# Kernel tuning notes

Measured on AMD Instinct MI355X. Metric: run time of the kernel, lower is better.

Reference implementation:

```python
import jax, jax.numpy as jnp
import numpy as np

B, C, H, W = 32, 3, 512, 512
EPS = 1e-8


def _radius_bins(h, w):
    cy, cx = h // 2, w // 2
    y = jnp.arange(h, dtype=jnp.float32) - cy
    x = jnp.arange(w, dtype=jnp.float32) - cx
    radius = jnp.sqrt(y[:, None] ** 2 + x[None, :] ** 2)  # [H, W]
    max_r = min(cy, cx)
    bins = jnp.floor(radius).astype(jnp.int32)
    # pixels with radius >= max_r fall outside all bins in the original loop;
    # route them to a dummy overflow bin that we drop afterwards.
    bins = jnp.where(bins < max_r, bins, max_r)
    return bins.reshape(-1), max_r


def _psd(x):
    f = jnp.fft.fft2(x)                  # over last two dims, like torch.fft.fft2
    psd = jnp.abs(f) ** 2
    return jnp.log(psd + EPS)            # log_power=True


def _radial_average(psd):
    b, c, h, w = psd.shape
    bins, max_r = _radius_bins(h, w)     # [H*W], static
    data = psd.reshape(b * c, h * w).T   # [H*W, B*C]
    sums = jax.ops.segment_sum(data, bins, num_segments=max_r + 1)
    counts = jax.ops.segment_sum(jnp.ones((h * w,), psd.dtype), bins,
                                 num_segments=max_r + 1)
    avg = jnp.where(counts[:, None] > 0, sums / counts[:, None], 0.0)
    avg = avg[:max_r]                    # drop overflow bin -> [max_r, B*C]
    return avg.T.reshape(b, c, max_r)


def setup_inputs() -> dict:
    key = jax.random.key(0)
    k1, k2 = jax.random.split(key)
    predicted = jax.random.normal(k1, (B, C, H, W), dtype=jnp.float32)
    target = jax.random.normal(k2, (B, C, H, W), dtype=jnp.float32)
    return {"predicted": predicted, "target": target}


def reference(predicted, target):
    pred_rad = _radial_average(_psd(predicted))
    targ_rad = _radial_average(_psd(target))
    return jnp.mean(jnp.abs(pred_rad - targ_rad))  # l1, reduction='mean'
```

## Files before the change

kernel.cpp:

```cpp
#include <hip/hip_runtime.h>
#include <math.h>

#define HH 512
#define WW 512
#define IMG (HH*WW)
#define NIMG_PER 96
#define NIMG 192
#define NBIN 256
#define EPSV 1e-8f
#define LN2F 0.69314718055994530942f

#define CSTR 264
#define IMGC (512*CSTR)
#define NTILE 33
#define SLOT 575

typedef float v2f __attribute__((ext_vector_type(2)));

__device__ __forceinline__ int drev(int s) {
    return ((s & 7) << 6) | (s & 56) | (s >> 6);
}
__device__ __forceinline__ int fsw(int a) { return a + (a >> 3); }

__device__ __forceinline__ v2f cmul(v2f a, v2f b) {
    return (v2f){a.x, a.x} * b + (v2f){a.y, a.y} * (v2f){-b.y, b.x};
}
__device__ __forceinline__ v2f cni(v2f a) { return (v2f){a.y, -a.x}; }

__device__ __forceinline__ void wsync() {
    asm volatile("" ::: "memory");
    __builtin_amdgcn_wave_barrier();
    asm volatile("" ::: "memory");
}

__device__ __forceinline__ void bfly8(v2f x[8]) {
    const float R = 0.70710678118654752440f;
    v2f t0=x[0]+x[4], t4=x[0]-x[4];
    v2f t1=x[1]+x[5], t5=x[1]-x[5];
    v2f t2=x[2]+x[6], t6=x[2]-x[6];
    v2f t3=x[3]+x[7], t7=x[3]-x[7];
    v2f u0=t0+t2, u2=t0-t2;
    v2f u1=t1+t3, u3=t1-t3;
    x[0]=u0+u1; x[4]=u0-u1;
    { v2f n3 = cni(u3); x[2]=u2+n3; x[6]=u2-n3; }
    v2f s1 = (v2f){R, R} * ((v2f){t5.x, t5.y} + (v2f){t5.y, -t5.x});
    v2f s2 = cni(t6);
    v2f s3 = (v2f){R, R} * ((v2f){t7.y, -t7.x} - (v2f){t7.x, t7.y});
    v2f v0=t4+s2, v2_=t4-s2;
    v2f v1=s1+s3, v3=s1-s3;
    x[1]=v0+v1; x[5]=v0-v1;
    { v2f m3 = cni(v3); x[3]=v2_+m3; x[7]=v2_-m3; }
}

__device__ __forceinline__ void twiddle7(v2f* x, float ang) {
    const float sn = __sinf(ang), cs = __cosf(ang);
    const v2f w1 = (v2f){cs, sn};
    const v2f w2 = cmul(w1, w1);
    const v2f w3 = cmul(w2, w1);
    const v2f w4 = cmul(w2, w2);
    const v2f w5 = cmul(w2, w3);
    const v2f w6 = cmul(w3, w3);
    const v2f w7 = cmul(w3, w4);
    x[1]=cmul(x[1],w1); x[2]=cmul(x[2],w2); x[3]=cmul(x[3],w3);
    x[4]=cmul(x[4],w4); x[5]=cmul(x[5],w5); x[6]=cmul(x[6],w6);
    x[7]=cmul(x[7],w7);
}

__global__ __launch_bounds__(512) void rowfft_kernel(
    const float* __restrict__ pred, const float* __restrict__ targ,
    v2f* __restrict__ out, int img_base)
{
    __shared__ v2f sd[8*SLOT];
    const int t    = threadIdx.x;
    const int lane = t & 63;
    const int w    = t >> 6;

    const int pb = blockIdx.x;
    const int li = blockIdx.y;
    const int g  = img_base + li;
    const float* img = (g < NIMG_PER) ? (pred + (size_t)g * IMG)
                                      : (targ + (size_t)(g - NIMG_PER) * IMG);
    const float* rowA = img + (size_t)(pb*16 + 2*w) * WW + lane;
    const float* rowB = rowA + WW;

    v2f* p = sd + w * SLOT;
    v2f x[8];
    const int i = lane;

    #pragma unroll
    for (int j = 0; j < 8; ++j)
        x[j] = (v2f){rowA[64*j], rowB[64*j]};
    bfly8(x);
    twiddle7(x, -0.012271846303085130f * (float)i);
    {
        v2f* q = p + fsw(i);
        #pragma unroll
        for (int j = 0; j < 8; ++j) q[72*j] = x[j];
    }
    wsync();

    {
        v2f* q = p + 72*(i >> 3) + (i & 7);
        #pragma unroll
        for (int j = 0; j < 8; ++j) x[j] = q[9*j];
        bfly8(x);
        twiddle7(x, -0.098174770424681038f * (float)(i & 7));
        #pragma unroll
        for (int j = 0; j < 8; ++j) q[9*j] = x[j];
    }
    wsync();

    {
        v2f* q = p + 9*i;
        #pragma unroll
        for (int j = 0; j < 8; ++j) x[j] = q[j];
        bfly8(x);
        #pragma unroll
        for (int j = 0; j < 8; ++j) q[j] = x[j];
    }
    wsync();

    v2f* dstA = out + (size_t)li * IMGC + (size_t)(pb*16 + 2*w) * CSTR;
    v2f* dstB = dstA + CSTR;
    #pragma unroll
    for (int it = 0; it < 5; ++it) {
        const int k = it*64 + lane;
        if (k <= 256) {
            const v2f P = p[fsw(drev(k))];
            const v2f Q = p[fsw(drev((512 - k) & 511))];
            dstA[k] = (v2f){0.5f, 0.5f} * (P + (v2f){Q.x, -Q.y});
            dstB[k] = (v2f){0.5f, 0.5f} * ((v2f){P.y, -P.x} + (v2f){Q.y, Q.x});
        } else if (k < CSTR) {
            dstA[k] = (v2f){0.0f, 0.0f};
            dstB[k] = (v2f){0.0f, 0.0f};
        }
    }
}

__global__ __launch_bounds__(512) void colfft_kernel(
    const v2f* __restrict__ in, float* __restrict__ bins2, int img_base)
{
    __shared__ v2f sd[8*SLOT];
    __shared__ float bs[4*257];
    const int t    = threadIdx.x;
    const int lane = t & 63;
    const int w    = t >> 6;

    for (int id = t; id < 4*257; id += 512) bs[id] = 0.0f;

    const int li = blockIdx.y;
    const int x0 = blockIdx.x * 8;
    {
        const int y0  = t >> 2;
        const int clp = t & 3;
        const float4* gsrc = (const float4*)(in + (size_t)li * IMGC + x0)
                           + (size_t)y0 * (CSTR/2) + clp;
        v2f* dA = sd + (2*clp)*SLOT + fsw(y0);
        v2f* dB = dA + SLOT;
        #pragma unroll
        for (int it = 0; it < 4; ++it) {
            const float4 v = gsrc[(size_t)it * 128 * (CSTR/2)];
            dA[144*it] = (v2f){v.x, v.y};
            dB[144*it] = (v2f){v.z, v.w};
        }
    }
    __syncthreads();

    v2f* p = sd + w * SLOT;
    v2f x[8];
    const int i = lane;

    {
        v2f* q = p + fsw(i);
        #pragma unroll
        for (int j = 0; j < 8; ++j) x[j] = q[72*j];
        bfly8(x);
        twiddle7(x, -0.012271846303085130f * (float)i);
        #pragma unroll
        for (int j = 0; j < 8; ++j) q[72*j] = x[j];
    }
    wsync();

    {
        v2f* q = p + 72*(i >> 3) + (i & 7);
        #pragma unroll
        for (int j = 0; j < 8; ++j) x[j] = q[9*j];
        bfly8(x);
        twiddle7(x, -0.098174770424681038f * (float)(i & 7));
        #pragma unroll
        for (int j = 0; j < 8; ++j) q[9*j] = x[j];
    }
    wsync();

    {
        v2f* q = p + 9*i;
        #pragma unroll
        for (int j = 0; j < 8; ++j) x[j] = q[j];
        bfly8(x);
        #pragma unroll
        for (int j = 0; j < 8; ++j) q[j] = x[j];
    }
    wsync();

    {
        const int h  = lane;
        const int kx = x0 + w;
        const bool valid = (kx <= 256);
        const float scale = (kx == 0 || kx == 256) ? 0.5f : 1.0f;
        const float dxf = (float)((kx - 256) * (kx - 256));
        float* bsw = bs + (w & 3) * 257;
        v2f* qb = p + fsw(8*(h & 7) + (h >> 3));
        float dyf = (float)(8*h - 256);

        float acc = 0.0f;
        int prevb = 1000;
        #pragma unroll
        for (int j = 0; j < 8; ++j) {
            const v2f v = qb[72*j];
            const float val = __log2f(fmaf(v.x, v.x, fmaf(v.y, v.y, EPSV)));
            const int b = (int)sqrtf(fmaf(dyf, dyf, dxf));
            dyf += 1.0f;
            if (b != prevb) {
                if (prevb < NBIN && valid) atomicAdd(&bsw[prevb], acc * scale);
                prevb = b; acc = val;
            } else {
                acc += val;
            }
        }
        if (prevb < NBIN && valid) atomicAdd(&bsw[prevb], acc * scale);
    }
    __syncthreads();

    if (t < NBIN) {
        float v = 0.0f;
        #pragma unroll
        for (int r = 0; r < 4; ++r) v += bs[r*257 + t];
        bins2[((size_t)blockIdx.x * NIMG + (img_base + li)) * NBIN + t] = 2.0f * v;
    }
}

__global__ __launch_bounds__(256) void reduce_kernel(
    const float* __restrict__ bins2, float* __restrict__ bins)
{
    const int li = blockIdx.x;
    const int t  = threadIdx.x;
    float s = 0.0f;
    #pragma unroll
    for (int tile = 0; tile < NTILE; ++tile)
        s += bins2[((size_t)tile * NIMG + li) * NBIN + t];
    bins[(size_t)li * NBIN + t] = s;
}

__global__ __launch_bounds__(256) void counts_kernel(float* __restrict__ cnt)
{
    __shared__ float c[NBIN];
    const int t = threadIdx.x;
    c[t] = 0.0f;
    __syncthreads();

    const int base = blockIdx.x * 4096;
    #pragma unroll
    for (int i = 0; i < 16; ++i) {
        const int id = base + i * 256 + t;
        const int y = id >> 9, xx = id & 511;
        const int dy = y - 256, dx = xx - 256;
        const int b  = (int)sqrtf((float)(dy*dy + dx*dx));
        if (b < NBIN) atomicAdd(&c[b], 1.0f);
    }
    __syncthreads();
    if (c[t] != 0.0f) atomicAdd(&cnt[t], c[t]);
}

__global__ __launch_bounds__(256) void finalize_kernel(
    const float* __restrict__ bins, const float* __restrict__ cnt,
    float* __restrict__ out)
{
    __shared__ float red[256];
    const int t = threadIdx.x;

    float acc = 0.0f;
    for (int id = t; id < NIMG_PER * NBIN; id += 256) {
        const int i = id >> 8;
        const int r = id & 255;
        const float d = fabsf(bins[(size_t)i * NBIN + r]
                            - bins[(size_t)(NIMG_PER + i) * NBIN + r]);
        acc += d / cnt[r];
    }
    red[t] = acc;
    __syncthreads();
    for (int w = 128; w > 0; w >>= 1) {
        if (t < w) red[t] += red[t + w];
        __syncthreads();
    }
    if (t == 0) out[0] = red[0] * (LN2F / (float)(NIMG_PER * NBIN));
}

extern "C" void kernel_launch(void* const* d_in, const int* in_sizes, int n_in,
                              void* d_out, int out_size, void* d_ws, size_t ws_size,
                              hipStream_t stream)
{
    const float* pred = (const float*)d_in[0];
    const float* targ = (const float*)d_in[1];
    float* out = (float*)d_out;

    char* ws = (char*)d_ws;
    float* cnt   = (float*)ws;
    float* bins  = cnt + NBIN;
    float* bins2 = bins + (size_t)NIMG * NBIN;
    const size_t fixed_f = NBIN + (size_t)NIMG*NBIN + (size_t)NTILE*NIMG*NBIN;
    const size_t off = (fixed_f*sizeof(float) + 255) & ~(size_t)255;
    v2f* cbuf = (v2f*)(ws + off);

    const size_t per_img = (size_t)IMGC * sizeof(v2f);
    size_t avail = (ws_size > off) ? (ws_size - off) : 0;
    int chunk = (int)(avail / per_img);
    if (chunk > NIMG) chunk = NIMG;
    if (chunk < 1) chunk = 1;

    hipMemsetAsync(cnt, 0, NBIN * sizeof(float), stream);
    counts_kernel<<<dim3(64), dim3(256), 0, stream>>>(cnt);

    for (int base = 0; base < NIMG; base += chunk) {
        const int n = (NIMG - base < chunk) ? (NIMG - base) : chunk;
        dim3 gA(HH / 16, n), gB(NTILE, n);
        rowfft_kernel<<<gA, dim3(512), 0, stream>>>(pred, targ, cbuf, base);
        colfft_kernel<<<gB, dim3(512), 0, stream>>>(cbuf, bins2, base);
    }

    reduce_kernel<<<dim3(NIMG), dim3(256), 0, stream>>>(bins2, bins);
    finalize_kernel<<<dim3(1), dim3(256), 0, stream>>>(bins, cnt, out);
}
```

Measured before the change: 225.6 us.

## Store row-FFT intermediate as packed fp16 and process two columns per wave

```diff
diff --git a/kernel.cpp b/kernel.cpp
--- a/kernel.cpp
+++ b/kernel.cpp
@@ -12,10 +12,11 @@
 
 #define CSTR 264
 #define IMGC (512*CSTR)
-#define NTILE 33
+#define NT16 17
 #define SLOT 575
 
-typedef float v2f __attribute__((ext_vector_type(2)));
+typedef float v2f  __attribute__((ext_vector_type(2)));
+typedef _Float16 h2f __attribute__((ext_vector_type(2)));
 
 __device__ __forceinline__ int drev(int s) {
     return ((s & 7) << 6) | (s & 56) | (s >> 6);
@@ -26,6 +27,14 @@
     return (v2f){a.x, a.x} * b + (v2f){a.y, a.y} * (v2f){-b.y, b.x};
 }
 __device__ __forceinline__ v2f cni(v2f a) { return (v2f){a.y, -a.x}; }
+
+__device__ __forceinline__ v2f h2tof(unsigned int u) {
+    h2f h = __builtin_bit_cast(h2f, u);
+    return (v2f){(float)h.x, (float)h.y};
+}
+__device__ __forceinline__ unsigned int ftoh2(v2f v) {
+    return __builtin_bit_cast(unsigned int, __builtin_amdgcn_cvt_pkrtz(v.x, v.y));
+}
 
 __device__ __forceinline__ void wsync() {
     asm volatile("" ::: "memory");
@@ -68,7 +77,7 @@
 
 __global__ __launch_bounds__(512) void rowfft_kernel(
     const float* __restrict__ pred, const float* __restrict__ targ,
-    v2f* __restrict__ out, int img_base)
+    unsigned int* __restrict__ out, int img_base)
 {
     __shared__ v2f sd[8*SLOT];
     const int t    = threadIdx.x;
@@ -120,27 +129,29 @@
     }
     wsync();
 
-    v2f* dstA = out + (size_t)li * IMGC + (size_t)(pb*16 + 2*w) * CSTR;
-    v2f* dstB = dstA + CSTR;
+    unsigned int* dstA = out + (size_t)li * IMGC + (size_t)(pb*16 + 2*w) * CSTR;
+    unsigned int* dstB = dstA + CSTR;
     #pragma unroll
     for (int it = 0; it < 5; ++it) {
         const int k = it*64 + lane;
         if (k <= 256) {
             const v2f P = p[fsw(drev(k))];
             const v2f Q = p[fsw(drev((512 - k) & 511))];
-            dstA[k] = (v2f){0.5f, 0.5f} * (P + (v2f){Q.x, -Q.y});
-            dstB[k] = (v2f){0.5f, 0.5f} * ((v2f){P.y, -P.x} + (v2f){Q.y, Q.x});
+            const v2f Fa = (v2f){0.5f, 0.5f} * (P + (v2f){Q.x, -Q.y});
+            const v2f Fb = (v2f){0.5f, 0.5f} * ((v2f){P.y, -P.x} + (v2f){Q.y, Q.x});
+            dstA[k] = ftoh2(Fa);
+            dstB[k] = ftoh2(Fb);
         } else if (k < CSTR) {
-            dstA[k] = (v2f){0.0f, 0.0f};
-            dstB[k] = (v2f){0.0f, 0.0f};
+            dstA[k] = 0u;
+            dstB[k] = 0u;
         }
     }
 }
 
 __global__ __launch_bounds__(512) void colfft_kernel(
-    const v2f* __restrict__ in, float* __restrict__ bins2, int img_base)
-{
-    __shared__ v2f sd[8*SLOT];
+    const unsigned int* __restrict__ in, float* __restrict__ bins2, int img_base)
+{
+    __shared__ unsigned int sd[16*SLOT];
     __shared__ float bs[4*257];
     const int t    = threadIdx.x;
     const int lane = t & 63;
@@ -149,85 +160,127 @@
     for (int id = t; id < 4*257; id += 512) bs[id] = 0.0f;
 
     const int li = blockIdx.y;
-    const int x0 = blockIdx.x * 8;
-    {
-        const int y0  = t >> 2;
-        const int clp = t & 3;
-        const float4* gsrc = (const float4*)(in + (size_t)li * IMGC + x0)
-                           + (size_t)y0 * (CSTR/2) + clp;
-        v2f* dA = sd + (2*clp)*SLOT + fsw(y0);
-        v2f* dB = dA + SLOT;
+    const int x0 = blockIdx.x * 16;
+    {
+        const int y0 = t >> 2;
+        const int c  = t & 3;
+        int cb = x0 + 4*c;
+        if (cb > CSTR - 4) cb = CSTR - 4;
+        const uint4* gsrc = (const uint4*)(in + (size_t)li * IMGC
+                                              + (size_t)y0 * CSTR + cb);
+        unsigned int* d0 = sd + (4*c + 0)*SLOT + fsw(y0);
+        unsigned int* d1 = d0 + SLOT;
+        unsigned int* d2 = d1 + SLOT;
+        unsigned int* d3 = d2 + SLOT;
         #pragma unroll
         for (int it = 0; it < 4; ++it) {
-            const float4 v = gsrc[(size_t)it * 128 * (CSTR/2)];
-            dA[144*it] = (v2f){v.x, v.y};
-            dB[144*it] = (v2f){v.z, v.w};
+            const uint4 v = gsrc[(size_t)it * 128 * (CSTR/4)];
+            d0[144*it] = v.x; d1[144*it] = v.y;
+            d2[144*it] = v.z; d3[144*it] = v.w;
         }
     }
     __syncthreads();
 
-    v2f* p = sd + w * SLOT;
-    v2f x[8];
+    unsigned int* pA = sd + (2*w)     * SLOT;
+    unsigned int* pB = sd + (2*w + 1) * SLOT;
+    v2f a[8], b[8];
     const int i = lane;
 
     {
-        v2f* q = p + fsw(i);
-        #pragma unroll
-        for (int j = 0; j < 8; ++j) x[j] = q[72*j];
-        bfly8(x);
-        twiddle7(x, -0.012271846303085130f * (float)i);
-        #pragma unroll
-        for (int j = 0; j < 8; ++j) q[72*j] = x[j];
-    }
-    wsync();
-
-    {
-        v2f* q = p + 72*(i >> 3) + (i & 7);
-        #pragma unroll
-        for (int j = 0; j < 8; ++j) x[j] = q[9*j];
-        bfly8(x);
-        twiddle7(x, -0.098174770424681038f * (float)(i & 7));
-        #pragma unroll
-        for (int j = 0; j < 8; ++j) q[9*j] = x[j];
-    }
-    wsync();
-
-    {
-        v2f* q = p + 9*i;
-        #pragma unroll
-        for (int j = 0; j < 8; ++j) x[j] = q[j];
-        bfly8(x);
-        #pragma unroll
-        for (int j = 0; j < 8; ++j) q[j] = x[j];
-    }
-    wsync();
-
-    {
-        const int h  = lane;
-        const int kx = x0 + w;
-        const bool valid = (kx <= 256);
-        const float scale = (kx == 0 || kx == 256) ? 0.5f : 1.0f;
-        const float dxf = (float)((kx - 256) * (kx - 256));
+        unsigned int* qA = pA + fsw(i);
+        unsigned int* qB = pB + fsw(i);
+        #pragma unroll
+        for (int j = 0; j < 8; ++j) { a[j] = h2tof(qA[72*j]); b[j] = h2tof(qB[72*j]); }
+        bfly8(a); bfly8(b);
+        const float ang = -0.012271846303085130f * (float)i;
+        const float sn = __sinf(ang), cs = __cosf(ang);
+        const v2f w1 = (v2f){cs, sn};
+        const v2f w2 = cmul(w1,w1), w3 = cmul(w2,w1), w4 = cmul(w2,w2);
+        const v2f w5 = cmul(w2,w3), w6 = cmul(w3,w3), w7 = cmul(w3,w4);
+        a[1]=cmul(a[1],w1); b[1]=cmul(b[1],w1);
+        a[2]=cmul(a[2],w2); b[2]=cmul(b[2],w2);
+        a[3]=cmul(a[3],w3); b[3]=cmul(b[3],w3);
+        a[4]=cmul(a[4],w4); b[4]=cmul(b[4],w4);
+        a[5]=cmul(a[5],w5); b[5]=cmul(b[5],w5);
+        a[6]=cmul(a[6],w6); b[6]=cmul(b[6],w6);
+        a[7]=cmul(a[7],w7); b[7]=cmul(b[7],w7);
+        #pragma unroll
+        for (int j = 0; j < 8; ++j) { qA[72*j] = ftoh2(a[j]); qB[72*j] = ftoh2(b[j]); }
+    }
+    wsync();
+
+    {
+        const int off = 72*(i >> 3) + (i & 7);
+        unsigned int* qA = pA + off;
+        unsigned int* qB = pB + off;
+        #pragma unroll
+        for (int j = 0; j < 8; ++j) { a[j] = h2tof(qA[9*j]); b[j] = h2tof(qB[9*j]); }
+        bfly8(a); bfly8(b);
+        const float ang = -0.098174770424681038f * (float)(i & 7);
+        const float sn = __sinf(ang), cs = __cosf(ang);
+        const v2f w1 = (v2f){cs, sn};
+        const v2f w2 = cmul(w1,w1), w3 = cmul(w2,w1), w4 = cmul(w2,w2);
+        const v2f w5 = cmul(w2,w3), w6 = cmul(w3,w3), w7 = cmul(w3,w4);
+        a[1]=cmul(a[1],w1); b[1]=cmul(b[1],w1);
+        a[2]=cmul(a[2],w2); b[2]=cmul(b[2],w2);
+        a[3]=cmul(a[3],w3); b[3]=cmul(b[3],w3);
+        a[4]=cmul(a[4],w4); b[4]=cmul(b[4],w4);
+        a[5]=cmul(a[5],w5); b[5]=cmul(b[5],w5);
+        a[6]=cmul(a[6],w6); b[6]=cmul(b[6],w6);
+        a[7]=cmul(a[7],w7); b[7]=cmul(b[7],w7);
+        #pragma unroll
+        for (int j = 0; j < 8; ++j) { qA[9*j] = ftoh2(a[j]); qB[9*j] = ftoh2(b[j]); }
+    }
+    wsync();
+
+    {
+        unsigned int* qA = pA + 9*i;
+        unsigned int* qB = pB + 9*i;
+        #pragma unroll
+        for (int j = 0; j < 8; ++j) { a[j] = h2tof(qA[j]); b[j] = h2tof(qB[j]); }
+        bfly8(a); bfly8(b);
+        #pragma unroll
+        for (int j = 0; j < 8; ++j) { qA[j] = ftoh2(a[j]); qB[j] = ftoh2(b[j]); }
+    }
+    wsync();
+
+    {
+        const int h   = lane;
+        const int kxA = x0 + 2*w;
+        const int kxB = kxA + 1;
+        const bool vA = (kxA <= 256), vB = (kxB <= 256);
+        const float sA = (kxA == 0 || kxA == 256) ? 0.5f : 1.0f;
+        const float sB = (kxB == 256) ? 0.5f : 1.0f;
+        const float dxA = (float)((kxA - 256) * (kxA - 256));
+        const float dxB = (float)((kxB - 256) * (kxB - 256));
         float* bsw = bs + (w & 3) * 257;
-        v2f* qb = p + fsw(8*(h & 7) + (h >> 3));
+        const int off = fsw(8*(h & 7) + (h >> 3));
+        unsigned int* qA = pA + off;
+        unsigned int* qB = pB + off;
         float dyf = (float)(8*h - 256);
 
-        float acc = 0.0f;
-        int prevb = 1000;
+        float accA = 0.0f, accB = 0.0f;
+        int pbA = 1000, pbB = 1000;
         #pragma unroll
         for (int j = 0; j < 8; ++j) {
-            const v2f v = qb[72*j];
-            const float val = __log2f(fmaf(v.x, v.x, fmaf(v.y, v.y, EPSV)));
-            const int b = (int)sqrtf(fmaf(dyf, dyf, dxf));
+            const v2f va = h2tof(qA[72*j]);
+            const v2f vb = h2tof(qB[72*j]);
+            const float la = __log2f(fmaf(va.x, va.x, fmaf(va.y, va.y, EPSV)));
+            const float lb = __log2f(fmaf(vb.x, vb.x, fmaf(vb.y, vb.y, EPSV)));
+            const int bA = (int)sqrtf(fmaf(dyf, dyf, dxA));
+            const int bB = (int)sqrtf(fmaf(dyf, dyf, dxB));
             dyf += 1.0f;
-            if (b != prevb) {
-                if (prevb < NBIN && valid) atomicAdd(&bsw[prevb], acc * scale);
-                prevb = b; acc = val;
-            } else {
-                acc += val;
-            }
+            if (bA != pbA) {
+                if (pbA < NBIN && vA) atomicAdd(&bsw[pbA], accA * sA);
+                pbA = bA; accA = la;
+            } else accA += la;
+            if (bB != pbB) {
+                if (pbB < NBIN && vB) atomicAdd(&bsw[pbB], accB * sB);
+                pbB = bB; accB = lb;
+            } else accB += lb;
         }
-        if (prevb < NBIN && valid) atomicAdd(&bsw[prevb], acc * scale);
+        if (pbA < NBIN && vA) atomicAdd(&bsw[pbA], accA * sA);
+        if (pbB < NBIN && vB) atomicAdd(&bsw[pbB], accB * sB);
     }
     __syncthreads();
 
@@ -246,7 +299,7 @@
     const int t  = threadIdx.x;
     float s = 0.0f;
     #pragma unroll
-    for (int tile = 0; tile < NTILE; ++tile)
+    for (int tile = 0; tile < NT16; ++tile)
         s += bins2[((size_t)tile * NIMG + li) * NBIN + t];
     bins[(size_t)li * NBIN + t] = s;
 }
@@ -307,11 +360,11 @@
     float* cnt   = (float*)ws;
     float* bins  = cnt + NBIN;
     float* bins2 = bins + (size_t)NIMG * NBIN;
-    const size_t fixed_f = NBIN + (size_t)NIMG*NBIN + (size_t)NTILE*NIMG*NBIN;
+    const size_t fixed_f = NBIN + (size_t)NIMG*NBIN + (size_t)NT16*NIMG*NBIN;
     const size_t off = (fixed_f*sizeof(float) + 255) & ~(size_t)255;
-    v2f* cbuf = (v2f*)(ws + off);
-
-    const size_t per_img = (size_t)IMGC * sizeof(v2f);
+    unsigned int* cbuf = (unsigned int*)(ws + off);
+
+    const size_t per_img = (size_t)IMGC * sizeof(unsigned int);
     size_t avail = (ws_size > off) ? (ws_size - off) : 0;
     int chunk = (int)(avail / per_img);
     if (chunk > NIMG) chunk = NIMG;
@@ -322,7 +375,7 @@
 
     for (int base = 0; base < NIMG; base += chunk) {
         const int n = (NIMG - base < chunk) ? (NIMG - base) : chunk;
-        dim3 gA(HH / 16, n), gB(NTILE, n);
+        dim3 gA(HH / 16, n), gB(NT16, n);
         rowfft_kernel<<<gA, dim3(512), 0, stream>>>(pred, targ, cbuf, base);
         colfft_kernel<<<gB, dim3(512), 0, stream>>>(cbuf, bins2, base);
     }
```

Result: faster. 212.9 us (-5.6%).
